# Kernel optimization log

Measured on AMD Instinct MI355X. Metric: run time of the kernel, lower is better.

The kernel has to match this reference:

```python
import jax, jax.numpy as jnp
import numpy as np

N_NODES = 80000
N_EDGES = 1280000
IN_C, HID_C, OUT_C = 128, 64, 40


def setup_inputs() -> dict:
    key = jax.random.key(0)
    k1, k2, k3, k4 = jax.random.split(key, 4)
    x = jax.random.normal(k1, (N_NODES, IN_C), dtype=jnp.float32)
    edge_index = jax.random.randint(k2, (2, N_EDGES), 0, N_NODES, dtype=jnp.int32)
    W1 = jax.random.normal(k3, (IN_C, HID_C), dtype=jnp.float32) * (1.0 / np.sqrt(IN_C))
    W2 = jax.random.normal(k4, (HID_C, OUT_C), dtype=jnp.float32) * (1.0 / np.sqrt(HID_C))
    return {"x": x, "edge_index": edge_index, "W1": W1, "W2": W2}


def _spmm_add(edge_index, h):
    # adj_t.matmul(h): out[dst] += h[src]  (aggr='add', message = x_j)
    src, dst = edge_index[0], edge_index[1]
    return jax.ops.segment_sum(h[src], dst, num_segments=N_NODES)


def reference(x, edge_index, W1, W2):
    # GCNConv 1: linear (no bias) then add-aggregate SpMM
    h = _spmm_add(edge_index, x @ W1)          # [N, HID]
    h = jax.nn.relu(h)
    # GCNConv 2
    h = _spmm_add(edge_index, h @ W2)          # [N, OUT]
    return jax.nn.log_softmax(h, axis=-1)
```

## Files before the change

kernel.cpp:

```cpp
#include <hip/hip_runtime.h>
#include <hip/hip_bf16.h>
#include <math.h>

#define N_NODES 80000
#define N_EDGES 1280000
#define IN_C 128
#define HID_C 64
#define OUT_C 40

#define KB 313
#define BK_CAP 4600
#define SEG 16
#define GCAP 416
#define BK2 (SEG * GCAP)
#define EPT_A 8
#define NBLK_A 313
#define NBLK_G1 625

__device__ __forceinline__ float bf_lo(unsigned u) {
    union { unsigned i; float f; } c; c.i = u << 16; return c.f;
}
__device__ __forceinline__ float bf_hi(unsigned u) {
    union { unsigned i; float f; } c; c.i = u & 0xffff0000u; return c.f;
}
__device__ __forceinline__ unsigned pack_bf2(float a, float b) {
    union { float f; unsigned i; } ca, cb; ca.f = a; cb.f = b;
    unsigned ra = (ca.i + 0x7fffu + ((ca.i >> 16) & 1u)) >> 16;
    unsigned rb = (cb.i + 0x7fffu + ((cb.i >> 16) & 1u)) >> 16;
    return ra | (rb << 16);
}

typedef short v8s __attribute__((ext_vector_type(8)));
typedef float v4f __attribute__((ext_vector_type(4)));
typedef float v2f __attribute__((ext_vector_type(2)));
union U16 { uint4 u; v8s s; };

__device__ __forceinline__ int wave_incl_scan(int v, int lane) {
#pragma unroll
    for (int o = 1; o < 64; o <<= 1) {
        const int t = __shfl_up(v, o, 64);
        if (lane >= o) v += t;
    }
    return v;
}

__global__ void prep_w_kernel(const float* __restrict__ W1, const float* __restrict__ W2,
                              unsigned* __restrict__ w1t, unsigned* __restrict__ w2t,
                              int* __restrict__ bcnt16) {
    const int g = blockIdx.x * 256 + threadIdx.x;
    if (g < SEG * KB) bcnt16[g] = 0;
    if (g < 4096) {
        const int wcol = g >> 6, kk = g & 63;
        w1t[g] = pack_bf2(W1[(2 * kk) * HID_C + wcol], W1[(2 * kk + 1) * HID_C + wcol]);
    }
    if (g < 1536) {
        const int wcol = g >> 5, kk = g & 31;
        w2t[g] = (wcol < OUT_C)
            ? pack_bf2(W2[(2 * kk) * OUT_C + wcol], W2[(2 * kk + 1) * OUT_C + wcol])
            : 0u;
    }
}

__global__ __launch_bounds__(512) void binA_gemm1_kernel(const int* __restrict__ src,
                                                         const int* __restrict__ dst,
                                                         int* __restrict__ bcnt16,
                                                         int* __restrict__ gbuf,
                                                         const float* __restrict__ x,
                                                         const unsigned* __restrict__ w1t,
                                                         unsigned* __restrict__ h1f) {
    if (blockIdx.x >= NBLK_A) {
        const int tid = threadIdx.x;
        const int wave = tid >> 6, lane = tid & 63;
        const int nl = lane & 15, quad = lane >> 4;
        const int node = ((blockIdx.x - NBLK_A) * 8 + wave) * 16 + nl;

        float4 xv[8];
#pragma unroll
        for (int kit = 0; kit < 4; ++kit) {
            const float* xp = x + (size_t)node * IN_C + kit * 32 + quad * 8;
            xv[kit * 2]     = *(const float4*)xp;
            xv[kit * 2 + 1] = *(const float4*)(xp + 4);
        }

        v4f acc[4];
#pragma unroll
        for (int q = 0; q < 4; ++q) acc[q] = (v4f){0.f, 0.f, 0.f, 0.f};

#pragma unroll
        for (int kit = 0; kit < 4; ++kit) {
            const float4 lo = xv[kit * 2], hi = xv[kit * 2 + 1];
            U16 bu;
            bu.u.x = pack_bf2(lo.x, lo.y); bu.u.y = pack_bf2(lo.z, lo.w);
            bu.u.z = pack_bf2(hi.x, hi.y); bu.u.w = pack_bf2(hi.z, hi.w);
#pragma unroll
            for (int mt = 0; mt < 4; ++mt) {
                U16 au;
                au.u = *(const uint4*)(w1t + ((mt * 16 + nl) * 64 + kit * 16 + quad * 4));
                acc[mt] = __builtin_amdgcn_mfma_f32_16x16x32_bf16(au.s, bu.s, acc[mt], 0, 0, 0);
            }
        }
#pragma unroll
        for (int mt = 0; mt < 4; ++mt) {
            int u = 0;
            u = __builtin_amdgcn_cvt_pk_fp8_f32(acc[mt][0], acc[mt][1], u, false);
            u = __builtin_amdgcn_cvt_pk_fp8_f32(acc[mt][2], acc[mt][3], u, true);
            h1f[(size_t)node * 16 + mt * 4 + quad] = (unsigned)u;
        }
        return;
    }

    __shared__ int lcnt[KB];
    __shared__ int lexcl[KB];
    __shared__ int lbase[KB];
    __shared__ int stage[512 * EPT_A];
    __shared__ int gaddr[512 * EPT_A];
    __shared__ int wss[8];
    __shared__ int total_s;
    const int tid = threadIdx.x;
    const int lane = tid & 63, wv = tid >> 6;
    const int gseg = blockIdx.x & (SEG - 1);

    for (int i = tid; i < KB; i += 512) lcnt[i] = 0;
    __syncthreads();

    const int e0 = blockIdx.x * 512 * EPT_A;
    int my_s[EPT_A], my_b[EPT_A], my_dl[EPT_A], my_r[EPT_A];
#pragma unroll
    for (int j = 0; j < EPT_A; ++j) {
        const int e = e0 + j * 512 + tid;
        if (e < N_EDGES) {
            const int d = dst[e];
            my_s[j] = src[e];
            my_b[j] = d >> 8;
            my_dl[j] = d & 255;
            my_r[j] = atomicAdd(&lcnt[my_b[j]], 1);
        } else my_b[j] = -1;
    }
    __syncthreads();

    {
        int v = (tid < KB) ? lcnt[tid] : 0;
        v = wave_incl_scan(v, lane);
        if (lane == 63) wss[wv] = v;
        __syncthreads();
        int pre = 0;
        for (int k = 0; k < wv; ++k) pre += wss[k];
        if (tid < KB) lexcl[tid] = v + pre;
        if (tid == KB - 1) total_s = v + pre;
        __syncthreads();
    }
    const int total = total_s;
    if (tid < KB) {
        lexcl[tid] -= lcnt[tid];
        lbase[tid] = (lcnt[tid] > 0) ? atomicAdd(&bcnt16[tid * SEG + gseg], lcnt[tid]) : 0;
    }
    __syncthreads();

#pragma unroll
    for (int j = 0; j < EPT_A; ++j) {
        if (my_b[j] >= 0) {
            const int b = my_b[j];
            const int li = lexcl[b] + my_r[j];
            stage[li] = (my_s[j] << 8) | my_dl[j];
            int gp = lbase[b] + my_r[j];
            if (gp >= GCAP) gp = GCAP - 1;
            gaddr[li] = b * BK2 + gseg * GCAP + gp;
        }
    }
    __syncthreads();

    for (int i = tid; i < total; i += 512)
        gbuf[gaddr[i]] = stage[i];
}

__global__ __launch_bounds__(512) void binB_g1_kernel(const int* __restrict__ bcnt16,
                                                      const int* __restrict__ gbuf,
                                                      const unsigned* __restrict__ h1f,
                                                      const unsigned* __restrict__ w2t,
                                                      int* __restrict__ rp,
                                                      int* __restrict__ col,
                                                      unsigned* __restrict__ h2f) {
    __shared__ int hist[256];
    __shared__ int excl[256];
    __shared__ int rp_l[260];
    __shared__ int outb[BK_CAP];
    __shared__ unsigned aggLds[256 * 36];
    __shared__ int ngs[SEG];
    __shared__ int wssA[8];
    __shared__ int wssB[8];
    __shared__ int cbase_s;
    const int b = blockIdx.x;
    const int tid = threadIdx.x;
    const int lane = tid & 63, wv = tid >> 6;

    int bv = 0;
    if (tid < KB) {
#pragma unroll
        for (int g = 0; g < SEG; ++g) bv += min(bcnt16[tid * SEG + g], GCAP);
        bv = min(bv, BK_CAP);
    }
    if (tid < 256) hist[tid] = 0;
    if (tid < SEG) ngs[tid] = min(bcnt16[b * SEG + tid], GCAP);
    {
        int iv = wave_incl_scan(bv, lane);
        if (lane == 63) wssA[wv] = iv;
        __syncthreads();
        int pre = 0;
        for (int k = 0; k < wv; ++k) pre += wssA[k];
        if (tid == b) cbase_s = iv + pre - bv;
        __syncthreads();
    }
    const int cbase = cbase_s;
    int n = 0;
#pragma unroll
    for (int g = 0; g < SEG; ++g) n += ngs[g];
    n = min(n, BK_CAP);
    const int* __restrict__ my = gbuf + (size_t)b * BK2;

    int my_pk[SEG], my_rk[SEG];
#pragma unroll
    for (int g = 0; g < SEG; ++g) {
        my_pk[g] = -1;
        if (tid < ngs[g]) {
            const int pk = my[g * GCAP + tid];
            my_pk[g] = pk;
            my_rk[g] = atomicAdd(&hist[pk & 255], 1);
        }
    }
    __syncthreads();

    {
        const int h = (tid < 256) ? hist[tid] : 0;
        int ih = wave_incl_scan(h, lane);
        if (lane == 63) wssB[wv] = ih;
        __syncthreads();
        int pre = 0;
        for (int k = 0; k < wv && k < 4; ++k) pre += wssB[k];
        if (tid < 256) {
            const int ex = ih + pre - h;
            excl[tid] = ex;
            rp_l[tid] = ex;
            const int node = b * 256 + tid;
            if (node <= N_NODES) rp[node] = cbase + ex;
        }
        if (tid == 256) rp_l[256] = n;
        __syncthreads();
    }

#pragma unroll
    for (int g = 0; g < SEG; ++g) {
        if (my_pk[g] >= 0) {
            const int pk = my_pk[g];
            const int pos = min(excl[pk & 255] + my_rk[g], BK_CAP - 1);
            outb[pos] = pk >> 8;
        }
    }
    __syncthreads();
    for (int i = tid; i < n; i += 512)
        col[cbase + i] = outb[i];

    const int sl8 = tid & 7;
    const int es = sl8 >> 2, cl = sl8 & 3;
#pragma unroll
    for (int p = 0; p < 4; ++p) {
        const int node_l = p * 64 + (tid >> 3);
        const int b0 = rp_l[node_l], e0 = rp_l[node_l + 1];

        v2f acc[8];
#pragma unroll
        for (int k = 0; k < 8; ++k) acc[k] = (v2f){0.f, 0.f};

        for (int pos = b0 + es; pos < e0; pos += 2) {
            const int s = outb[pos];
            const uint4 v = *(const uint4*)(h1f + (size_t)s * 16 + cl * 4);
            acc[0] += __builtin_amdgcn_cvt_pk_f32_fp8((int)v.x, false);
            acc[1] += __builtin_amdgcn_cvt_pk_f32_fp8((int)v.x, true);
            acc[2] += __builtin_amdgcn_cvt_pk_f32_fp8((int)v.y, false);
            acc[3] += __builtin_amdgcn_cvt_pk_f32_fp8((int)v.y, true);
            acc[4] += __builtin_amdgcn_cvt_pk_f32_fp8((int)v.z, false);
            acc[5] += __builtin_amdgcn_cvt_pk_f32_fp8((int)v.z, true);
            acc[6] += __builtin_amdgcn_cvt_pk_f32_fp8((int)v.w, false);
            acc[7] += __builtin_amdgcn_cvt_pk_f32_fp8((int)v.w, true);
        }
#pragma unroll
        for (int k = 0; k < 8; ++k) {
#pragma unroll
            for (int h = 0; h < 2; ++h)
                acc[k][h] += __shfl_down(acc[k][h], 4, 64);
        }
        if (sl8 < 4) {
            unsigned o8[8];
#pragma unroll
            for (int t = 0; t < 8; ++t) {
                const int k = 2 * (t >> 1) + (t & 1);
                o8[t] = pack_bf2(fmaxf(acc[k][0], 0.f), fmaxf(acc[k][1], 0.f));
            }
            uint4 w0, w1;
            w0.x = o8[0]; w0.y = o8[1]; w0.z = o8[2]; w0.w = o8[3];
            w1.x = o8[4]; w1.y = o8[5]; w1.z = o8[6]; w1.w = o8[7];
            *(uint4*)(aggLds + node_l * 36 + cl * 8) = w0;
            *(uint4*)(aggLds + node_l * 36 + cl * 8 + 4) = w1;
        }
    }
    __syncthreads();

    const int wave = tid >> 6;
    const int nl = lane & 15, quad = lane >> 4;
#pragma unroll
    for (int it = 0; it < 2; ++it) {
        const int node_l = (wave * 2 + it) * 16 + nl;
        const int node2 = b * 256 + node_l;

        v4f c[3];
#pragma unroll
        for (int m = 0; m < 3; ++m) c[m] = (v4f){0.f, 0.f, 0.f, 0.f};

#pragma unroll
        for (int kit = 0; kit < 2; ++kit) {
            U16 bu;
            bu.u = *(const uint4*)(aggLds + node_l * 36 + kit * 16 + quad * 4);
#pragma unroll
            for (int mt = 0; mt < 3; ++mt) {
                U16 au;
                au.u = *(const uint4*)(w2t + ((mt * 16 + nl) * 32 + kit * 16 + quad * 4));
                c[mt] = __builtin_amdgcn_mfma_f32_16x16x32_bf16(au.s, bu.s, c[mt], 0, 0, 0);
            }
        }
        if (node2 < N_NODES) {
#pragma unroll
            for (int mt = 0; mt < 3; ++mt) {
                const int idx = mt * 4 + quad;
                if (idx < 10) {
                    int u = 0;
                    u = __builtin_amdgcn_cvt_pk_fp8_f32(c[mt][0], c[mt][1], u, false);
                    u = __builtin_amdgcn_cvt_pk_fp8_f32(c[mt][2], c[mt][3], u, true);
                    h2f[(size_t)node2 * 10 + idx] = (unsigned)u;
                }
            }
        }
    }
}

__global__ void gather40_ls_kernel(const int* __restrict__ rp, const int* __restrict__ col,
                                   const unsigned* __restrict__ h2f,
                                   float* __restrict__ out) {
    __shared__ int lcol[1024];
    const int tid = threadIdx.x;
    const int lane = tid & 63;
    const int wave = tid >> 6;
    const int sl = lane & 15;
    const int es = sl / 5;
    const int cl = sl - es * 5;
    const int gbase = lane & 48;
    const int nb = blockIdx.x * 16;

    const int seg_b = rp[nb];
    const int seg_n = min(rp[nb + 16] - seg_b, 1024);
    for (int i = tid; i < seg_n; i += 256) lcol[i] = col[seg_b + i];
    __syncthreads();

    const int node = nb + wave * 4 + (lane >> 4);
    const int b = rp[node], e = rp[node + 1];

    v2f a[4];
#pragma unroll
    for (int k = 0; k < 4; ++k) a[k] = (v2f){0.f, 0.f};

    for (int pos = b; __any(pos < e); pos += 24) {
#pragma unroll
        for (int j = 0; j < 8; ++j) {
            const int ei = pos + j * 3 + es;
            if ((es < 3) && (ei < e)) {
                const int o = ei - seg_b;
                const int s = (o < seg_n) ? lcol[o] : col[ei];
                const uint2 v = *(const uint2*)(h2f + (size_t)s * 10 + cl * 2);
                a[0] += __builtin_amdgcn_cvt_pk_f32_fp8((int)v.x, false);
                a[1] += __builtin_amdgcn_cvt_pk_f32_fp8((int)v.x, true);
                a[2] += __builtin_amdgcn_cvt_pk_f32_fp8((int)v.y, false);
                a[3] += __builtin_amdgcn_cvt_pk_f32_fp8((int)v.y, true);
            }
        }
    }
#pragma unroll
    for (int k = 0; k < 4; ++k) {
#pragma unroll
        for (int h = 0; h < 2; ++h) {
            const float u = __shfl_down(a[k][h], 5, 64);
            const float w = __shfl_down(a[k][h], 10, 64);
            a[k][h] += u + w;
        }
    }

    const bool own = sl < 5;
    float m = -INFINITY;
    if (own) {
#pragma unroll
        for (int k = 0; k < 4; ++k) m = fmaxf(m, fmaxf(a[k][0], a[k][1]));
    }
    const float m0 = __shfl(m, gbase + 0, 64), m1 = __shfl(m, gbase + 1, 64);
    const float m2 = __shfl(m, gbase + 2, 64), m3 = __shfl(m, gbase + 3, 64);
    const float m4 = __shfl(m, gbase + 4, 64);
    const float gm = fmaxf(fmaxf(fmaxf(m0, m1), fmaxf(m2, m3)), m4);

    float s = 0.f;
    if (own) {
#pragma unroll
        for (int k = 0; k < 4; ++k)
            s += __expf(a[k][0] - gm) + __expf(a[k][1] - gm);
    }
    const float s0 = __shfl(s, gbase + 0, 64), s1 = __shfl(s, gbase + 1, 64);
    const float s2 = __shfl(s, gbase + 2, 64), s3 = __shfl(s, gbase + 3, 64);
    const float s4 = __shfl(s, gbase + 4, 64);
    const float ls = __logf(s0 + s1 + s2 + s3 + s4) + gm;

    if (own) {
        float* op = out + (size_t)node * OUT_C + cl * 8;
        *(float4*)op = make_float4(a[0][0] - ls, a[0][1] - ls, a[1][0] - ls, a[1][1] - ls);
        *(float4*)(op + 4) = make_float4(a[2][0] - ls, a[2][1] - ls, a[3][0] - ls, a[3][1] - ls);
    }
}

extern "C" void kernel_launch(void* const* d_in, const int* in_sizes, int n_in,
                              void* d_out, int out_size, void* d_ws, size_t ws_size,
                              hipStream_t stream) {
    const float* x  = (const float*)d_in[0];
    const int* eidx = (const int*)d_in[1];
    const float* W1 = (const float*)d_in[2];
    const float* W2 = (const float*)d_in[3];
    float* out = (float*)d_out;

    const int* src = eidx;
    const int* dst = eidx + N_EDGES;

    unsigned* h1f    = (unsigned*)d_ws;
    unsigned* h2f    = h1f + (size_t)N_NODES * 16;
    int*      gbuf   = (int*)(h2f + (size_t)N_NODES * 10);
    int*      col    = gbuf + (size_t)KB * BK2;
    int*      rp     = col + N_EDGES;
    int*      bcnt16 = rp + 80004;
    unsigned* w1t    = (unsigned*)(bcnt16 + SEG * KB + 8);
    unsigned* w2t    = w1t + 4096;

    prep_w_kernel<<<20, 256, 0, stream>>>(W1, W2, w1t, w2t, bcnt16);
    binA_gemm1_kernel<<<NBLK_A + NBLK_G1, 512, 0, stream>>>(src, dst, bcnt16, gbuf, x, w1t, h1f);

    binB_g1_kernel<<<KB, 512, 0, stream>>>(bcnt16, gbuf, h1f, w2t, rp, col, h2f);
    gather40_ls_kernel<<<N_NODES / 16, 256, 0, stream>>>(rp, col, h2f, out);
}
```

Measured before the change: 164.9 us.

## Split each binB bucket across two blocks, duplicating the CSR build

The binB_g1 kernel now launches two blocks per 256-node bucket. Both blocks rebuild the bucket's local CSR sort redundantly, but each aggregates and runs the second GEMM for only 128 nodes, and only one block writes rp and col. The aim is more blocks in flight (626 instead of 313) on a GPU with many CUs, plus half the aggregation LDS per block. The cost is doubled gbuf reads, histogram and scatter work per bucket.

```diff
diff --git a/kernel.cpp b/kernel.cpp
--- a/kernel.cpp
+++ b/kernel.cpp
@@ -184,12 +184,13 @@
     __shared__ int excl[256];
     __shared__ int rp_l[260];
     __shared__ int outb[BK_CAP];
-    __shared__ unsigned aggLds[256 * 36];
+    __shared__ unsigned aggLds[128 * 36];
     __shared__ int ngs[SEG];
     __shared__ int wssA[8];
     __shared__ int wssB[8];
     __shared__ int cbase_s;
-    const int b = blockIdx.x;
+    const int bb = blockIdx.x >> 1;
+    const int half = blockIdx.x & 1;
     const int tid = threadIdx.x;
     const int lane = tid & 63, wv = tid >> 6;
 
@@ -200,14 +201,14 @@
         bv = min(bv, BK_CAP);
     }
     if (tid < 256) hist[tid] = 0;
-    if (tid < SEG) ngs[tid] = min(bcnt16[b * SEG + tid], GCAP);
+    if (tid < SEG) ngs[tid] = min(bcnt16[bb * SEG + tid], GCAP);
     {
         int iv = wave_incl_scan(bv, lane);
         if (lane == 63) wssA[wv] = iv;
         __syncthreads();
         int pre = 0;
         for (int k = 0; k < wv; ++k) pre += wssA[k];
-        if (tid == b) cbase_s = iv + pre - bv;
+        if (tid == bb) cbase_s = iv + pre - bv;
         __syncthreads();
     }
     const int cbase = cbase_s;
@@ -215,7 +216,7 @@
 #pragma unroll
     for (int g = 0; g < SEG; ++g) n += ngs[g];
     n = min(n, BK_CAP);
-    const int* __restrict__ my = gbuf + (size_t)b * BK2;
+    const int* __restrict__ my = gbuf + (size_t)bb * BK2;
 
     int my_pk[SEG], my_rk[SEG];
 #pragma unroll
@@ -240,8 +241,8 @@
             const int ex = ih + pre - h;
             excl[tid] = ex;
             rp_l[tid] = ex;
-            const int node = b * 256 + tid;
-            if (node <= N_NODES) rp[node] = cbase + ex;
+            const int node = bb * 256 + tid;
+            if (half == 0 && node <= N_NODES) rp[node] = cbase + ex;
         }
         if (tid == 256) rp_l[256] = n;
         __syncthreads();
@@ -256,14 +257,17 @@
         }
     }
     __syncthreads();
-    for (int i = tid; i < n; i += 512)
-        col[cbase + i] = outb[i];
+    if (half == 0) {
+        for (int i = tid; i < n; i += 512)
+            col[cbase + i] = outb[i];
+    }
 
     const int sl8 = tid & 7;
     const int es = sl8 >> 2, cl = sl8 & 3;
 #pragma unroll
-    for (int p = 0; p < 4; ++p) {
-        const int node_l = p * 64 + (tid >> 3);
+    for (int p = 0; p < 2; ++p) {
+        const int l = p * 64 + (tid >> 3);
+        const int node_l = half * 128 + l;
         const int b0 = rp_l[node_l], e0 = rp_l[node_l + 1];
 
         v2f acc[8];
@@ -298,18 +302,17 @@
             uint4 w0, w1;
             w0.x = o8[0]; w0.y = o8[1]; w0.z = o8[2]; w0.w = o8[3];
             w1.x = o8[4]; w1.y = o8[5]; w1.z = o8[6]; w1.w = o8[7];
-            *(uint4*)(aggLds + node_l * 36 + cl * 8) = w0;
-            *(uint4*)(aggLds + node_l * 36 + cl * 8 + 4) = w1;
+            *(uint4*)(aggLds + l * 36 + cl * 8) = w0;
+            *(uint4*)(aggLds + l * 36 + cl * 8 + 4) = w1;
         }
     }
     __syncthreads();
 
     const int wave = tid >> 6;
     const int nl = lane & 15, quad = lane >> 4;
-#pragma unroll
-    for (int it = 0; it < 2; ++it) {
-        const int node_l = (wave * 2 + it) * 16 + nl;
-        const int node2 = b * 256 + node_l;
+    {
+        const int l = wave * 16 + nl;
+        const int node2 = bb * 256 + half * 128 + l;
 
         v4f c[3];
 #pragma unroll
@@ -318,7 +321,7 @@
 #pragma unroll
         for (int kit = 0; kit < 2; ++kit) {
             U16 bu;
-            bu.u = *(const uint4*)(aggLds + node_l * 36 + kit * 16 + quad * 4);
+            bu.u = *(const uint4*)(aggLds + l * 36 + kit * 16 + quad * 4);
 #pragma unroll
             for (int mt = 0; mt < 3; ++mt) {
                 U16 au;
@@ -444,6 +447,6 @@
     prep_w_kernel<<<20, 256, 0, stream>>>(W1, W2, w1t, w2t, bcnt16);
     binA_gemm1_kernel<<<NBLK_A + NBLK_G1, 512, 0, stream>>>(src, dst, bcnt16, gbuf, x, w1t, h1f);
 
-    binB_g1_kernel<<<KB, 512, 0, stream>>>(bcnt16, gbuf, h1f, w2t, rp, col, h2f);
+    binB_g1_kernel<<<2 * KB, 512, 0, stream>>>(bcnt16, gbuf, h1f, w2t, rp, col, h2f);
     gather40_ls_kernel<<<N_NODES / 16, 256, 0, stream>>>(rp, col, h2f, out);
 }
```

After: 157.8 us, median of 2. 4.3% less time.
